# Kernel tuning notes

Hardware: AMD Instinct MI355X
Metric: run time of the kernel (lower is better)

## Reference

```python
import jax, jax.numpy as jnp
import numpy as np

B, NA, NM, P, IN, H, OUT = 64, 49, 19, 128, 64, 64, 60
H2 = 2 * H  # feature dim after each GCN concat and for the global GAT


def setup_inputs() -> dict:
    key = jax.random.key(0)
    ks = iter(jax.random.split(key, 64))
    def rn(shape, s=0.05):
        return jax.random.normal(next(ks), shape, jnp.float32) * s
    inp = {
        'agent_feature': jax.random.normal(next(ks), (B, NA, IN), jnp.float32),
        'map_feature': jax.random.normal(next(ks), (P, B, NM, IN), jnp.float32),
        'map_mask': jnp.ones((B, P), jnp.int32),
    }
    for pfx in ('a', 'm'):  # agent / map SubNetwork params, 3 layers each
        dims = [IN, H2, H2]
        for i in range(3):
            inp[f'{pfx}w{i}'] = rn((dims[i], H))
            inp[f'{pfx}b{i}'] = jnp.zeros((H,), jnp.float32)
            inp[f'{pfx}g{i}'] = jnp.ones((H,), jnp.float32)   # LayerNorm gamma
            inp[f'{pfx}n{i}'] = jnp.zeros((H,), jnp.float32)  # LayerNorm beta
    inp['gat_fc_w'] = rn((H2, H2))
    inp['gat_attn_w'] = rn((2 * H2,))  # attn_fc over concat([z_src, z_dst])
    inp['mlp_w'] = rn((H2, OUT))
    inp['mlp_b'] = jnp.zeros((OUT,), jnp.float32)
    return inp


def _layer_norm(x, g, b):
    mu = jnp.mean(x, axis=-1, keepdims=True)
    var = jnp.mean((x - mu) ** 2, axis=-1, keepdims=True)
    return g * (x - mu) / jnp.sqrt(var + 1e-5) + b


def _neighbor_max(h):
    # max over all OTHER nodes of a complete digraph (no self loop).
    # top-2 trick per channel avoids materializing an [N,N,D] mailbox.
    top2 = jax.lax.top_k(jnp.swapaxes(h, -1, -2), 2)[0]  # [..., D, 2]
    m1 = top2[..., 0][..., None, :]  # [..., 1, D] global max
    m2 = top2[..., 1][..., None, :]  # [..., 1, D] second max
    return jnp.where(h == m1, m2, m1)


def _subnet(x, params):
    for W, b, g, be in params:
        h = jax.nn.relu(_layer_norm(x @ W + b, g, be))
        x = jnp.concatenate([h, _neighbor_max(h)], axis=-1)
    return x


def _forward(agent_feature, map_feature, ap, mp, gat_fc_w, gat_attn_w, mlp_w, mlp_b):
    a = _subnet(agent_feature, ap)        # [B, NA, 2H]
    m = _subnet(map_feature, mp)          # [P, B, NM, 2H]
    agent_poly = jnp.max(a, axis=1)       # [B, 2H]
    map_poly = jnp.max(m, axis=2)         # [P, B, 2H]
    feats = jnp.concatenate([agent_poly[None], map_poly], axis=0)  # [1+P, B, 2H]
    feats = jnp.swapaxes(feats, 0, 1)     # [B, Nn, 2H], node 0 = agent
    z = feats @ gat_fc_w                  # [B, Nn, 2H]
    s = z @ gat_attn_w[:H2]               # [B, Nn] source contribution
    d = z @ gat_attn_w[H2:]               # [B, Nn] destination contribution
    e = jax.nn.leaky_relu(s[:, :, None] + d[:, None, :], 0.01)  # edge i->j: [B, i, j]
    nn_ = feats.shape[1]
    e = jnp.where(jnp.eye(nn_, dtype=bool)[None], -jnp.inf, e)  # no self edges
    alpha = jax.nn.softmax(e, axis=1)     # segment softmax over sources per dst
    hg = jnp.einsum('bij,bid->bjd', alpha, z)  # weighted-sum message passing
    return hg[:, 0] @ mlp_w + mlp_b       # agent node readout: [B, OUT]


def reference(agent_feature, map_feature, map_mask,
              aw0, ab0, ag0, an0, aw1, ab1, ag1, an1, aw2, ab2, ag2, an2,
              mw0, mb0, mg0, mn0, mw1, mb1, mg1, mn1, mw2, mb2, mg2, mn2,
              gat_fc_w, gat_attn_w, mlp_w, mlp_b):
    del map_mask  # all-ones mask => all P map polylines participate (static)
    ap = [(aw0, ab0, ag0, an0), (aw1, ab1, ag1, an1), (aw2, ab2, ag2, an2)]
    mp = [(mw0, mb0, mg0, mn0), (mw1, mb1, mg1, mn1), (mw2, mb2, mg2, mn2)]
    return _forward(agent_feature, map_feature, ap, mp, gat_fc_w, gat_attn_w, mlp_w, mlp_b)
```

## Files before the change

### kernel.cpp

```cpp
#include <hip/hip_runtime.h>
#include <stdint.h>

#define B_    64
#define NA_   49
#define NM_   19
#define P_    128
#define OUT_  60
#define AGRID 32
#define MGRID 1366
#define XR     128
#define XBYTES (XR * 256)
#define WBBYTES 16384
#define PBYTES (9 * 64 * 4)
#define SMEMB  (XBYTES + WBBYTES + PBYTES)
#define FEATS_BYTES (129 * 64 * 128 * 4)

typedef __bf16 bf16x8 __attribute__((ext_vector_type(8)));
typedef float  f32x16 __attribute__((ext_vector_type(16)));
typedef unsigned short ushort_t;

__device__ __forceinline__ unsigned int cvt_pk_bf16(float lo, float hi) {
  unsigned int r;
  asm("v_cvt_pk_bf16_f32 %0, %1, %2" : "=v"(r) : "v"(lo), "v"(hi));
  return r;
}

__device__ __forceinline__ f32x16 zero16() {
  f32x16 z;
#pragma unroll
  for (int i = 0; i < 16; ++i) z[i] = 0.f;
  return z;
}

__device__ __forceinline__ int xswz(int row, int byteoff) {
  return row * 256 + (byteoff ^ ((row & 7) << 4));
}

template<int KS>
__device__ __forceinline__ void stage_w_direct(const float* __restrict__ W,
                                               char* __restrict__ wbuf) {
  const int nfrag = KS * 128;
  for (int f = threadIdx.x; f < nfrag; f += 256) {
    int g = f >> 6, s = f & 63;
    int ks = g >> 1, mt = g & 1;
    int hi = s & 1, lr = s >> 1;
    const float* src = W + (ks * 16 + hi * 8) * 64 + (mt * 32 + lr);
    uint4 u;
    u.x = cvt_pk_bf16(src[0],   src[64]);
    u.y = cvt_pk_bf16(src[128], src[192]);
    u.z = cvt_pk_bf16(src[256], src[320]);
    u.w = cvt_pk_bf16(src[384], src[448]);
    *(uint4*)(wbuf + f * 16) = u;
  }
}

template<int KS>
__device__ __forceinline__ void tile_layer(
    const char* __restrict__ wl,
    char* __restrict__ xs, int xrow0, int vr,
    const float* __restrict__ Pb, const float* __restrict__ Pg,
    const float* __restrict__ Pn)
{
  const int lane = threadIdx.x & 63;
  const int lr   = lane & 31;
  const int hi   = lane >> 5;
  const int ch4  = hi * 4;
  const int br   = xrow0 + lr;
  const int wo   = (lr * 2 + hi) * 16;

  bf16x8 bfr[KS];
#pragma unroll
  for (int ks = 0; ks < KS; ++ks)
    bfr[ks] = *(const bf16x8*)(xs + xswz(br, ks * 32 + hi * 16));

  f32x16 acc0 = zero16(), acc1 = zero16();
#pragma unroll
  for (int ks = 0; ks < KS; ++ks) {
    bf16x8 a0 = *(const bf16x8*)(wl + (ks * 2 + 0) * 1024 + wo);
    bf16x8 a1 = *(const bf16x8*)(wl + (ks * 2 + 1) * 1024 + wo);
    acc0 = __builtin_amdgcn_mfma_f32_32x32x16_bf16(a0, bfr[ks], acc0, 0, 0, 0);
    acc1 = __builtin_amdgcn_mfma_f32_32x32x16_bf16(a1, bfr[ks], acc1, 0, 0, 0);
  }

#pragma unroll
  for (int b = 0; b < 4; ++b) {
    float4 t0 = *(const float4*)&Pb[8 * b + ch4];
    float4 t1 = *(const float4*)&Pb[32 + 8 * b + ch4];
    acc0[4*b+0] += t0.x; acc0[4*b+1] += t0.y;
    acc0[4*b+2] += t0.z; acc0[4*b+3] += t0.w;
    acc1[4*b+0] += t1.x; acc1[4*b+1] += t1.y;
    acc1[4*b+2] += t1.z; acc1[4*b+3] += t1.w;
  }
  float s = 0.f, q = 0.f;
#pragma unroll
  for (int r = 0; r < 16; ++r) {
    s += acc0[r] + acc1[r];
    q = fmaf(acc0[r], acc0[r], q);
    q = fmaf(acc1[r], acc1[r], q);
  }
  s += __shfl_xor(s, 32);
  q += __shfl_xor(q, 32);
  float mu   = s * 0.015625f;
  float rstd = rsqrtf(fmaf(q, 0.015625f, -mu * mu) + 1e-5f);

#pragma unroll
  for (int b = 0; b < 4; ++b) {
    float4 g0 = *(const float4*)&Pg[8 * b + ch4];
    float4 n0 = *(const float4*)&Pn[8 * b + ch4];
    float4 g1 = *(const float4*)&Pg[32 + 8 * b + ch4];
    float4 n1 = *(const float4*)&Pn[32 + 8 * b + ch4];
    float h00 = fmaxf(0.f, fmaf((acc0[4*b+0] - mu) * rstd, g0.x, n0.x));
    float h01 = fmaxf(0.f, fmaf((acc0[4*b+1] - mu) * rstd, g0.y, n0.y));
    float h02 = fmaxf(0.f, fmaf((acc0[4*b+2] - mu) * rstd, g0.z, n0.z));
    float h03 = fmaxf(0.f, fmaf((acc0[4*b+3] - mu) * rstd, g0.w, n0.w));
    float h10 = fmaxf(0.f, fmaf((acc1[4*b+0] - mu) * rstd, g1.x, n1.x));
    float h11 = fmaxf(0.f, fmaf((acc1[4*b+1] - mu) * rstd, g1.y, n1.y));
    float h12 = fmaxf(0.f, fmaf((acc1[4*b+2] - mu) * rstd, g1.z, n1.z));
    float h13 = fmaxf(0.f, fmaf((acc1[4*b+3] - mu) * rstd, g1.w, n1.w));
    if (lr < vr) {
      uint2 u0; u0.x = cvt_pk_bf16(h00, h01); u0.y = cvt_pk_bf16(h02, h03);
      uint2 u1; u1.x = cvt_pk_bf16(h10, h11); u1.y = cvt_pk_bf16(h12, h13);
      *(uint2*)(xs + xswz(br, 16 * b + 8 * hi)) = u0;
      *(uint2*)(xs + xswz(br, 64 + 16 * b + 8 * hi)) = u1;
    }
  }
}

__device__ __forceinline__ void nmax_one(char* xs, int g, int c) {
  const int rb = g * NM_;
  unsigned int xv[NM_];
  unsigned int m1 = 0, m2 = 0;
#pragma unroll
  for (int n = 0; n < NM_; ++n) {
    xv[n] = *(const ushort_t*)(xs + xswz(rb + n, 2 * c));
    if (xv[n] > m1) { m2 = m1; m1 = xv[n]; } else if (xv[n] > m2) m2 = xv[n];
  }
#pragma unroll
  for (int n = 0; n < NM_; ++n)
    *(ushort_t*)(xs + xswz(rb + n, 128 + 2 * c)) =
        (ushort_t)((xv[n] == m1) ? m2 : m1);
}

__device__ __forceinline__ void nmax_agent2(char* xs) {
  const int tid = threadIdx.x;
  if (tid >= 128) return;
  const int g = tid >> 6, c = tid & 63;
  const int rb = g * 64;
  unsigned int m1 = 0, m2 = 0;
  for (int n = 0; n < NA_; ++n) {
    unsigned int x = *(const ushort_t*)(xs + xswz(rb + n, 2 * c));
    if (x > m1) { m2 = m1; m1 = x; } else if (x > m2) m2 = x;
  }
  for (int n = 0; n < NA_; ++n) {
    unsigned int x = *(const ushort_t*)(xs + xswz(rb + n, 2 * c));
    *(ushort_t*)(xs + xswz(rb + n, 128 + 2 * c)) =
        (ushort_t)((x == m1) ? m2 : m1);
  }
}

__device__ __forceinline__ void stage_params(
    const float* b0, const float* g0, const float* n0,
    const float* b1, const float* g1, const float* n1,
    const float* b2, const float* g2, const float* n2, float* Pp)
{
  const int tid = threadIdx.x;
  if (tid < 64) {
    Pp[      tid] = b0[tid]; Pp[ 64 + tid] = g0[tid]; Pp[128 + tid] = n0[tid];
    Pp[192 + tid] = b1[tid]; Pp[256 + tid] = g1[tid]; Pp[320 + tid] = n1[tid];
    Pp[384 + tid] = b2[tid]; Pp[448 + tid] = g2[tid]; Pp[512 + tid] = n2[tid];
  }
}

__global__ __launch_bounds__(256, 3) void subnet16(
    const float* __restrict__ agent, const float* __restrict__ mapf,
    const float* __restrict__ aw0, const float* __restrict__ ab0,
    const float* __restrict__ ag0, const float* __restrict__ an0,
    const float* __restrict__ aw1, const float* __restrict__ ab1,
    const float* __restrict__ ag1, const float* __restrict__ an1,
    const float* __restrict__ aw2, const float* __restrict__ ab2,
    const float* __restrict__ ag2, const float* __restrict__ an2,
    const float* __restrict__ mw0, const float* __restrict__ mb0,
    const float* __restrict__ mg0, const float* __restrict__ mn0,
    const float* __restrict__ mw1, const float* __restrict__ mb1,
    const float* __restrict__ mg1, const float* __restrict__ mn1,
    const float* __restrict__ mw2, const float* __restrict__ mb2,
    const float* __restrict__ mg2, const float* __restrict__ mn2,
    const float* __restrict__ fcw, const float* __restrict__ attnw,
    float* __restrict__ feats, float* __restrict__ waswad)
{
  __shared__ __align__(16) char smem[SMEMB];
  char*  xs   = smem;
  char*  wbuf = smem + XBYTES;
  float* Pp   = (float*)(smem + XBYTES + WBBYTES);
  const int tid = threadIdx.x;
  const int wid = tid >> 6;

  if (blockIdx.x == AGRID + MGRID) {
    const int lane = tid & 63;
    float a0 = attnw[lane],       a1 = attnw[64 + lane];
    float dd0 = attnw[128 + lane], dd1 = attnw[192 + lane];
    for (int r = wid; r < 128; r += 4) {
      float w0 = fcw[r * 128 + lane], w1 = fcw[r * 128 + 64 + lane];
      float s1 = w0 * a0 + w1 * a1;
      float s2 = w0 * dd0 + w1 * dd1;
#pragma unroll
      for (int off = 32; off; off >>= 1) {
        s1 += __shfl_xor(s1, off);
        s2 += __shfl_xor(s2, off);
      }
      if (lane == 0) { waswad[r] = s1; waswad[128 + r] = s2; }
    }
    return;
  }

  if (blockIdx.x < AGRID) {
    const int bid = blockIdx.x;
    const int vr = (wid & 1) ? 17 : 32;
    for (int i = tid; i < 2 * NA_ * 16; i += 256) {
      int g = i / (NA_ * 16);
      int rem = i - g * (NA_ * 16);
      int row = rem >> 4, k4 = (rem & 15) * 4;
      float4 v = *(const float4*)&agent[((size_t)(2 * bid + g) * NA_ + row) * 64 + k4];
      uint2 u; u.x = cvt_pk_bf16(v.x, v.y); u.y = cvt_pk_bf16(v.z, v.w);
      *(uint2*)(xs + xswz(g * 64 + row, 8 * (rem & 15))) = u;
    }
    stage_w_direct<4>(aw0, wbuf);
    stage_params(ab0, ag0, an0, ab1, ag1, an1, ab2, ag2, an2, Pp);
    __syncthreads();
    tile_layer<4>(wbuf, xs, wid * 32, vr, Pp, Pp + 64, Pp + 128);
    __syncthreads();
    nmax_agent2(xs);
    stage_w_direct<8>(aw1, wbuf);
    __syncthreads();
    tile_layer<8>(wbuf, xs, wid * 32, vr, Pp + 192, Pp + 256, Pp + 320);
    __syncthreads();
    nmax_agent2(xs);
    stage_w_direct<8>(aw2, wbuf);
    __syncthreads();
    tile_layer<8>(wbuf, xs, wid * 32, vr, Pp + 384, Pp + 448, Pp + 512);
    __syncthreads();
    if (tid < 128) {
      const int g = tid >> 6, c = tid & 63;
      const int rb = g * 64;
      unsigned int m1 = 0;
      for (int n = 0; n < NA_; ++n) {
        unsigned int x = *(const ushort_t*)(xs + xswz(rb + n, 2 * c));
        m1 = x > m1 ? x : m1;
      }
      float f = __uint_as_float(m1 << 16);
      size_t slot = (size_t)(2 * bid + g);
      feats[slot * 128 + c] = f;
      feats[slot * 128 + 64 + c] = f;
    }
  } else {
    const int mbid = blockIdx.x - AGRID;
    const int gbase = mbid * 6;
    const int ng = (gbase + 6 <= P_ * B_) ? 6 : (P_ * B_ - gbase);
    const int rows = ng * NM_;
    int vr = rows - wid * 32;
    vr = vr > 32 ? 32 : vr;
    for (int i = tid; i < rows * 16; i += 256) {
      int row = i >> 4, k4 = (i & 15) * 4;
      float4 v = *(const float4*)&mapf[((size_t)gbase * NM_ + row) * 64 + k4];
      uint2 u; u.x = cvt_pk_bf16(v.x, v.y); u.y = cvt_pk_bf16(v.z, v.w);
      *(uint2*)(xs + xswz(row, 8 * (i & 15))) = u;
    }
    stage_w_direct<4>(mw0, wbuf);
    stage_params(mb0, mg0, mn0, mb1, mg1, mn1, mb2, mg2, mn2, Pp);
    __syncthreads();
    if (vr > 0) tile_layer<4>(wbuf, xs, wid * 32, vr, Pp, Pp + 64, Pp + 128);
    __syncthreads();
    for (int i = tid; i < ng * 64; i += 256) nmax_one(xs, i >> 6, i & 63);
    stage_w_direct<8>(mw1, wbuf);
    __syncthreads();
    if (vr > 0) tile_layer<8>(wbuf, xs, wid * 32, vr,
                              Pp + 192, Pp + 256, Pp + 320);
    __syncthreads();
    for (int i = tid; i < ng * 64; i += 256) nmax_one(xs, i >> 6, i & 63);
    stage_w_direct<8>(mw2, wbuf);
    __syncthreads();
    if (vr > 0) tile_layer<8>(wbuf, xs, wid * 32, vr,
                              Pp + 384, Pp + 448, Pp + 512);
    __syncthreads();
    for (int i = tid; i < ng * 64; i += 256) {
      const int g = i >> 6, c = i & 63;
      const int rb = g * NM_;
      unsigned int m1 = 0;
      for (int n = 0; n < NM_; ++n) {
        unsigned int x = *(const ushort_t*)(xs + xswz(rb + n, 2 * c));
        m1 = x > m1 ? x : m1;
      }
      float f = __uint_as_float(m1 << 16);
      size_t slot = (size_t)(B_ + gbase + g);
      feats[slot * 128 + c] = f;
      feats[slot * 128 + 64 + c] = f;
    }
  }
}

__global__ __launch_bounds__(256) void gat_kernel(
    const float* __restrict__ feats,
    const float* __restrict__ fcw,
    const float* __restrict__ waswad,
    const float* __restrict__ mlpw,
    const float* __restrict__ mlpb,
    float* __restrict__ out)
{
  const int b = blockIdx.x, tid = threadIdx.x;
  __shared__ float was[128], wad[128];
  __shared__ float si[130];
  __shared__ float alpha[128], red[8];
  __shared__ float up[2][128], ubuf[128], hgp[2][128], op[2][60];

  if (tid < 128) { was[tid] = waswad[tid]; wad[tid] = waswad[128 + tid]; }
  __syncthreads();

  {
    const int idx = tid >> 1, half = tid & 1;
    const float* fr = feats + ((size_t)(idx + 1) * B_ + b) * 128 + half * 64;
    const float* wa = was + half * 64;
    float s = 0.f;
    for (int k = 0; k < 64; k += 4) {
      float4 f = *(const float4*)&fr[k];
      s += f.x * wa[k] + f.y * wa[k + 1] + f.z * wa[k + 2] + f.w * wa[k + 3];
    }
    s += __shfl_xor(s, 1);
    if (half == 0) si[idx + 1] = s;
    if (tid < 2) {
      const float* f0 = feats + (size_t)b * 128 + tid * 64;
      const float* wd = wad + tid * 64;
      float s2 = 0.f;
      for (int k = 0; k < 64; k += 4) {
        float4 f = *(const float4*)&f0[k];
        s2 += f.x * wd[k] + f.y * wd[k + 1] + f.z * wd[k + 2] + f.w * wd[k + 3];
      }
      s2 += __shfl_xor(s2, 1);
      if (tid == 0) si[129] = s2;
    }
  }
  __syncthreads();

  float d0 = si[129];
  float e = -3.4e38f;
  if (tid < 128) {
    float x = si[tid + 1] + d0;
    e = (x > 0.f) ? x : 0.01f * x;
  }
  float m = e;
#pragma unroll
  for (int off = 32; off; off >>= 1) m = fmaxf(m, __shfl_xor(m, off));
  if ((tid & 63) == 0) red[tid >> 6] = m;
  __syncthreads();
  float mx = fmaxf(red[0], red[1]);
  float p = (tid < 128) ? expf(e - mx) : 0.f;
  float s = p;
#pragma unroll
  for (int off = 32; off; off >>= 1) s += __shfl_xor(s, off);
  if ((tid & 63) == 0) red[4 + (tid >> 6)] = s;
  __syncthreads();
  float denom = red[4] + red[5];
  if (tid < 128) alpha[tid] = p / denom;
  __syncthreads();

  {
    const int c = tid & 127, h = tid >> 7;
    const float* fb = feats + ((size_t)(h * 64 + 1) * B_ + b) * 128 + c;
    float u = 0.f;
    for (int t = 0; t < 64; ++t)
      u += alpha[h * 64 + t] * fb[(size_t)t * B_ * 128];
    up[h][c] = u;
  }
  __syncthreads();
  if (tid < 128) ubuf[tid] = up[0][tid] + up[1][tid];
  __syncthreads();

  {
    const int c = tid & 127, h = tid >> 7;
    float sacc = 0.f;
    for (int k = 0; k < 64; ++k)
      sacc += ubuf[h * 64 + k] * fcw[(h * 64 + k) * 128 + c];
    hgp[h][c] = sacc;
  }
  __syncthreads();

  if (tid < 120) {
    const int o = tid % 60, h = tid / 60;
    float sacc = 0.f;
    for (int c = 0; c < 64; ++c)
      sacc += (hgp[0][h * 64 + c] + hgp[1][h * 64 + c]) * mlpw[(h * 64 + c) * OUT_ + o];
    op[h][o] = sacc;
  }
  __syncthreads();
  if (tid < OUT_) out[b * OUT_ + tid] = mlpb[tid] + op[0][tid] + op[1][tid];
}

extern "C" void kernel_launch(void* const* d_in, const int* in_sizes, int n_in,
                              void* d_out, int out_size, void* d_ws, size_t ws_size,
                              hipStream_t stream) {
  (void)in_sizes; (void)n_in; (void)out_size; (void)ws_size;

  const float* agent = (const float*)d_in[0];
  const float* mapf  = (const float*)d_in[1];

  const float* aw0 = (const float*)d_in[3];
  const float* ab0 = (const float*)d_in[4];
  const float* ag0 = (const float*)d_in[5];
  const float* an0 = (const float*)d_in[6];
  const float* aw1 = (const float*)d_in[7];
  const float* ab1 = (const float*)d_in[8];
  const float* ag1 = (const float*)d_in[9];
  const float* an1 = (const float*)d_in[10];
  const float* aw2 = (const float*)d_in[11];
  const float* ab2 = (const float*)d_in[12];
  const float* ag2 = (const float*)d_in[13];
  const float* an2 = (const float*)d_in[14];

  const float* mw0 = (const float*)d_in[15];
  const float* mb0 = (const float*)d_in[16];
  const float* mg0 = (const float*)d_in[17];
  const float* mn0 = (const float*)d_in[18];
  const float* mw1 = (const float*)d_in[19];
  const float* mb1 = (const float*)d_in[20];
  const float* mg1 = (const float*)d_in[21];
  const float* mn1 = (const float*)d_in[22];
  const float* mw2 = (const float*)d_in[23];
  const float* mb2 = (const float*)d_in[24];
  const float* mg2 = (const float*)d_in[25];
  const float* mn2 = (const float*)d_in[26];

  const float* fcw   = (const float*)d_in[27];
  const float* attnw = (const float*)d_in[28];
  const float* mlpw  = (const float*)d_in[29];
  const float* mlpb  = (const float*)d_in[30];

  float* feats = (float*)d_ws;
  float* waswad = (float*)((char*)d_ws + FEATS_BYTES);
  float* out = (float*)d_out;

  subnet16<<<AGRID + MGRID + 1, 256, 0, stream>>>(
      agent, mapf,
      aw0, ab0, ag0, an0, aw1, ab1, ag1, an1, aw2, ab2, ag2, an2,
      mw0, mb0, mg0, mn0, mw1, mb1, mg1, mn1, mw2, mb2, mg2, mn2,
      fcw, attnw, feats, waswad);

  gat_kernel<<<B_, 256, 0, stream>>>(feats, fcw, waswad, mlpw, mlpb, out);
}
```

Before: 51.12 us.

## Process map polylines per-wave with all layer weights resident in LDS

Map blocks now stage all three layer weight matrices once into a larger shared buffer and loop over 16 polylines per block, with each wave independently handling four polylines through all three layers and the neighbor-max steps. This removes the block-wide barriers between layers and reduces repeated weight staging across many small blocks. In exchange, the larger LDS footprint lowers occupancy (launch bounds drop to 2 blocks per SM), and each wave's 19-row tile underuses the 32-row MFMA tiles.

```diff
diff --git a/kernel.cpp b/kernel.cpp
--- a/kernel.cpp
+++ b/kernel.cpp
@@ -7,10 +7,11 @@
 #define P_    128
 #define OUT_  60
 #define AGRID 32
-#define MGRID 1366
+#define MGRID 512
+#define GPW   4
 #define XR     128
 #define XBYTES (XR * 256)
-#define WBBYTES 16384
+#define WBBYTES 40960
 #define PBYTES (9 * 64 * 4)
 #define SMEMB  (XBYTES + WBBYTES + PBYTES)
 #define FEATS_BYTES (129 * 64 * 128 * 4)
@@ -126,8 +127,8 @@
   }
 }
 
-__device__ __forceinline__ void nmax_one(char* xs, int g, int c) {
-  const int rb = g * NM_;
+__device__ __forceinline__ void nmax_wave19(char* xs, int rb) {
+  const int c = threadIdx.x & 63;
   unsigned int xv[NM_];
   unsigned int m1 = 0, m2 = 0;
 #pragma unroll
@@ -171,7 +172,7 @@
   }
 }
 
-__global__ __launch_bounds__(256, 3) void subnet16(
+__global__ __launch_bounds__(256, 2) void subnet17(
     const float* __restrict__ agent, const float* __restrict__ mapf,
     const float* __restrict__ aw0, const float* __restrict__ ab0,
     const float* __restrict__ ag0, const float* __restrict__ an0,
@@ -254,46 +255,39 @@
     }
   } else {
     const int mbid = blockIdx.x - AGRID;
-    const int gbase = mbid * 6;
-    const int ng = (gbase + 6 <= P_ * B_) ? 6 : (P_ * B_ - gbase);
-    const int rows = ng * NM_;
-    int vr = rows - wid * 32;
-    vr = vr > 32 ? 32 : vr;
-    for (int i = tid; i < rows * 16; i += 256) {
-      int row = i >> 4, k4 = (i & 15) * 4;
-      float4 v = *(const float4*)&mapf[((size_t)gbase * NM_ + row) * 64 + k4];
-      uint2 u; u.x = cvt_pk_bf16(v.x, v.y); u.y = cvt_pk_bf16(v.z, v.w);
-      *(uint2*)(xs + xswz(row, 8 * (i & 15))) = u;
-    }
+    const int gbase = mbid * 16;
     stage_w_direct<4>(mw0, wbuf);
+    stage_w_direct<8>(mw1, wbuf + 8192);
+    stage_w_direct<8>(mw2, wbuf + 24576);
     stage_params(mb0, mg0, mn0, mb1, mg1, mn1, mb2, mg2, mn2, Pp);
     __syncthreads();
-    if (vr > 0) tile_layer<4>(wbuf, xs, wid * 32, vr, Pp, Pp + 64, Pp + 128);
-    __syncthreads();
-    for (int i = tid; i < ng * 64; i += 256) nmax_one(xs, i >> 6, i & 63);
-    stage_w_direct<8>(mw1, wbuf);
-    __syncthreads();
-    if (vr > 0) tile_layer<8>(wbuf, xs, wid * 32, vr,
-                              Pp + 192, Pp + 256, Pp + 320);
-    __syncthreads();
-    for (int i = tid; i < ng * 64; i += 256) nmax_one(xs, i >> 6, i & 63);
-    stage_w_direct<8>(mw2, wbuf);
-    __syncthreads();
-    if (vr > 0) tile_layer<8>(wbuf, xs, wid * 32, vr,
-                              Pp + 384, Pp + 448, Pp + 512);
-    __syncthreads();
-    for (int i = tid; i < ng * 64; i += 256) {
-      const int g = i >> 6, c = i & 63;
-      const int rb = g * NM_;
-      unsigned int m1 = 0;
-      for (int n = 0; n < NM_; ++n) {
-        unsigned int x = *(const ushort_t*)(xs + xswz(rb + n, 2 * c));
-        m1 = x > m1 ? x : m1;
+
+    const int lane = tid & 63;
+    const int wb = wid * 20;
+    for (int it = 0; it < GPW; ++it) {
+      const int gidx = gbase + wid * GPW + it;
+      for (int i = lane; i < NM_ * 16; i += 64) {
+        int row = i >> 4, k4 = (i & 15) * 4;
+        float4 v = *(const float4*)&mapf[((size_t)gidx * NM_ + row) * 64 + k4];
+        uint2 u; u.x = cvt_pk_bf16(v.x, v.y); u.y = cvt_pk_bf16(v.z, v.w);
+        *(uint2*)(xs + xswz(wb + row, 8 * (i & 15))) = u;
       }
-      float f = __uint_as_float(m1 << 16);
-      size_t slot = (size_t)(B_ + gbase + g);
-      feats[slot * 128 + c] = f;
-      feats[slot * 128 + 64 + c] = f;
+      tile_layer<4>(wbuf, xs, wb, NM_, Pp, Pp + 64, Pp + 128);
+      nmax_wave19(xs, wb);
+      tile_layer<8>(wbuf + 8192, xs, wb, NM_, Pp + 192, Pp + 256, Pp + 320);
+      nmax_wave19(xs, wb);
+      tile_layer<8>(wbuf + 24576, xs, wb, NM_, Pp + 384, Pp + 448, Pp + 512);
+      {
+        unsigned int m1 = 0;
+        for (int n = 0; n < NM_; ++n) {
+          unsigned int x = *(const ushort_t*)(xs + xswz(wb + n, 2 * lane));
+          m1 = x > m1 ? x : m1;
+        }
+        float f = __uint_as_float(m1 << 16);
+        float* dst = feats + (size_t)(B_ + gidx) * 128;
+        dst[lane] = f;
+        dst[64 + lane] = f;
+      }
     }
   }
 }
@@ -437,7 +431,7 @@
   float* waswad = (float*)((char*)d_ws + FEATS_BYTES);
   float* out = (float*)d_out;
 
-  subnet16<<<AGRID + MGRID + 1, 256, 0, stream>>>(
+  subnet17<<<AGRID + MGRID + 1, 256, 0, stream>>>(
       agent, mapf,
       aw0, ab0, ag0, an0, aw1, ab1, ag1, an1, aw2, ab2, ag2, an2,
       mw0, mb0, mg0, mn0, mw1, mb1, mg1, mn1, mw2, mb2, mg2, mn2,
```

New measurement: 60.15 us. 17.7% more time.
